# Kernel optimization log

Measured on AMD Instinct MI355X. Metric: run time of the kernel, lower is better.

Reference implementation:

```python
import jax, jax.numpy as jnp
import numpy as np

NEG_INF = -1e30  # stand-in for float('-inf') that is softmax-safe


def setup_inputs() -> dict:
    key = jax.random.key(0)
    ks = jax.random.split(key, 6)
    B, H, S, D = 2, 8, 1024, 64
    NF, K = 4, 3
    return {
        "query": jax.random.normal(ks[0], (B, H, S, D), dtype=jnp.float32),
        "keys": jax.random.normal(ks[1], (B, H, S, D), dtype=jnp.float32),
        "vals": jax.random.normal(ks[2], (B, H, S, D), dtype=jnp.float32),
        "mask": jnp.ones((B, 1, S, S), dtype=jnp.int32),
        "conv_w": jax.random.normal(ks[3], (NF, 1, K, K), dtype=jnp.float32) * (1.0 / K),
        "conv_b": jnp.zeros((NF,), dtype=jnp.float32),
        "lin_w": jax.random.normal(ks[4], (1, NF), dtype=jnp.float32) * 0.5,
        "lin_b": jnp.zeros((1,), dtype=jnp.float32),
    }


def reference(query, keys, vals, mask, conv_w, conv_b, lin_w, lin_b):
    B, H, S, D = query.shape
    NF = conv_w.shape[0]
    K = conv_w.shape[2]
    scale = jnp.asarray(D, query.dtype) ** 0.5

    # [B,H,S,S] raw dot-product scores
    dp = jnp.einsum("bhsd,bhtd->bhst", query, keys) / scale

    # conv2d over the score matrix: treat (B*H) as batch, 1 input channel
    x = dp.reshape(B * H, 1, S, S)
    conv = jax.lax.conv_general_dilated(
        x, conv_w,
        window_strides=(1, 1),
        padding=[(K // 2, K // 2), (K // 2, K // 2)],
        dimension_numbers=("NCHW", "OIHW", "NCHW"),
    ) + conv_b[None, :, None, None]
    conv = jax.nn.leaky_relu(conv, negative_slope=0.01)  # [B*H, NF, S, S]

    # per-pixel linear over the filter axis (Linear(num_filters, 1))
    conv = conv.reshape(B, H, NF, S, S)
    preattn = jnp.einsum("bhfst,f->bhst", conv, lin_w[0]) + lin_b[0]

    # masking + softmax (mask broadcasts over heads)
    preattn = jnp.where(mask == 0, jnp.asarray(NEG_INF, preattn.dtype), preattn)
    attn = jax.nn.softmax(preattn, axis=-1)

    # dropout is identity in eval mode
    return jnp.einsum("bhst,bhtd->bhsd", attn, vals)
```

## Files before the change

kernel.cpp:

```cpp
#include <hip/hip_runtime.h>
#include <math.h>

#define S_LEN 1024
#define D_DIM 64
#define NBH   16

typedef unsigned short ushort_t;
typedef __attribute__((ext_vector_type(8))) short short8;
typedef __attribute__((ext_vector_type(4))) short short4v;
typedef __attribute__((ext_vector_type(4))) float f32x4;
typedef __attribute__((ext_vector_type(2))) float f32x2;

__device__ __forceinline__ ushort_t rne_bf16(float x) {
    unsigned u = __float_as_uint(x);
    return (ushort_t)((u + 0x7FFFu + ((u >> 16) & 1u)) >> 16);
}
__device__ __forceinline__ void split1(float x, ushort_t& h, ushort_t& l) {
    h = rne_bf16(x);
    float hf = __uint_as_float((unsigned)h << 16);
    l = rne_bf16(x - hf);
}

__global__ __launch_bounds__(256) void prep(
    const float* __restrict__ k, const float* __restrict__ v,
    const int* __restrict__ mask,
    ushort_t* __restrict__ khi, ushort_t* __restrict__ klo,
    ushort_t* __restrict__ vhi, ushort_t* __restrict__ vlo,
    unsigned* __restrict__ mw)
{
    __shared__ float Ls[64][65];
    const int tid = threadIdx.x;
    const int bx = blockIdx.x;
    if (bx < 512) {
        const int gid  = bx * 256 + tid;
        const int bh   = gid >> 13;
        const int tile = (gid >> 7) & 63;
        const int ch   = (gid >> 6) & 1;
        const int lane = gid & 63;
        const int quad = lane >> 4, t15 = lane & 15;
        const float* src = k + ((size_t)bh * S_LEN + tile * 16 + t15) * D_DIM
                             + ch * 32 + quad * 8;
        float x[8];
        *(float4*)(x + 0) = *(const float4*)(src);
        *(float4*)(x + 4) = *(const float4*)(src + 4);
        short8 hv, lv;
        #pragma unroll
        for (int i = 0; i < 8; ++i) {
            ushort_t h, l;
            split1(x[i], h, l);
            hv[i] = (short)h; lv[i] = (short)l;
        }
        *(short8*)(khi + (size_t)gid * 8) = hv;
        *(short8*)(klo + (size_t)gid * 8) = lv;
    } else if (bx < 768) {
        const int bi = bx - 512;
        const int tt = bi & 15, bh = bi >> 4;
        const float* vb = v + ((size_t)bh * S_LEN + tt * 64) * D_DIM;
        #pragma unroll
        for (int p = 0; p < 4; ++p) {
            int idx = p * 1024 + tid * 4;
            int r = idx >> 6, c = idx & 63;
            float4 x = *(const float4*)(vb + r * 64 + c);
            Ls[r][c] = x.x; Ls[r][c+1] = x.y; Ls[r][c+2] = x.z; Ls[r][c+3] = x.w;
        }
        __syncthreads();
        const int d = tid >> 2, c0 = (tid & 3) * 16;
        ushort_t hi[16], lo[16];
        #pragma unroll
        for (int j = 0; j < 16; ++j) split1(Ls[c0 + j][d], hi[j], lo[j]);
        const int tb0 = tt * 8 + (c0 >> 3);
        const size_t o0 = (((size_t)bh * 128 + tb0) * 64 + d) * 8;
        const size_t o1 = (((size_t)bh * 128 + tb0 + 1) * 64 + d) * 8;
        *(short8*)(vhi + o0) = *(short8*)(hi);
        *(short8*)(vhi + o1) = *(short8*)(hi + 8);
        *(short8*)(vlo + o0) = *(short8*)(lo);
        *(short8*)(vlo + o1) = *(short8*)(lo + 8);
    } else {
        const int gid = (bx - 768) * 256 + tid;
        const int row = gid >> 5, wd = gid & 31;
        const int4* mp = (const int4*)(mask + (size_t)row * 1024 + wd * 32);
        unsigned bits = 0;
        #pragma unroll
        for (int p = 0; p < 8; ++p) {
            int4 qv = mp[p];
            bits |= (qv.x != 0 ? 1u : 0u) << (p * 4 + 0);
            bits |= (qv.y != 0 ? 1u : 0u) << (p * 4 + 1);
            bits |= (qv.z != 0 ? 1u : 0u) << (p * 4 + 2);
            bits |= (qv.w != 0 ? 1u : 0u) << (p * 4 + 3);
        }
        mw[(size_t)row * 32 + wd] = bits;
    }
}

__global__ __launch_bounds__(256) void qk_mfma(
    const float* __restrict__ q,
    const ushort_t* __restrict__ khi, const ushort_t* __restrict__ klo,
    float* __restrict__ dp)
{
    const int strip = blockIdx.x, st = blockIdx.y, bh = blockIdx.z;
    const int s0 = st * 16;
    const int tid = threadIdx.x;
    const int wave = tid >> 6, lane = tid & 63;
    const int m = lane & 15, quad = lane >> 4;

    const float* qp = q + ((size_t)bh * S_LEN + s0 + m) * D_DIM + quad * 8;
    float qa[16];
    *(float4*)(qa + 0)  = *(const float4*)(qp + 0);
    *(float4*)(qa + 4)  = *(const float4*)(qp + 4);
    *(float4*)(qa + 8)  = *(const float4*)(qp + 32);
    *(float4*)(qa + 12) = *(const float4*)(qp + 36);
    short8 ahi0, alo0, ahi1, alo1;
    #pragma unroll
    for (int i = 0; i < 8; ++i) {
        ushort_t h, l;
        split1(qa[i], h, l);      ahi0[i] = (short)h; alo0[i] = (short)l;
        split1(qa[8 + i], h, l);  ahi1[i] = (short)h; alo1[i] = (short)l;
    }

    const int tile0 = strip * 16 + wave * 4;
    float* dpb = dp + ((size_t)bh * S_LEN + s0) * S_LEN;
    #pragma unroll
    for (int tt = 0; tt < 4; ++tt) {
        const int tile = tile0 + tt;
        const size_t kb = ((size_t)bh * 8192 + tile * 128) + lane;
        short8 bhi0 = *(const short8*)(khi + kb * 8);
        short8 blo0 = *(const short8*)(klo + kb * 8);
        short8 bhi1 = *(const short8*)(khi + (kb + 64) * 8);
        short8 blo1 = *(const short8*)(klo + (kb + 64) * 8);
        f32x4 acc = {0.f, 0.f, 0.f, 0.f};
        acc = __builtin_amdgcn_mfma_f32_16x16x32_bf16(ahi0, bhi0, acc, 0, 0, 0);
        acc = __builtin_amdgcn_mfma_f32_16x16x32_bf16(ahi0, blo0, acc, 0, 0, 0);
        acc = __builtin_amdgcn_mfma_f32_16x16x32_bf16(alo0, bhi0, acc, 0, 0, 0);
        acc = __builtin_amdgcn_mfma_f32_16x16x32_bf16(ahi1, bhi1, acc, 0, 0, 0);
        acc = __builtin_amdgcn_mfma_f32_16x16x32_bf16(ahi1, blo1, acc, 0, 0, 0);
        acc = __builtin_amdgcn_mfma_f32_16x16x32_bf16(alo1, bhi1, acc, 0, 0, 0);
        const int t0 = tile * 16;
        #pragma unroll
        for (int r = 0; r < 4; ++r)
            dpb[(size_t)(quad * 4 + r) * S_LEN + t0 + m] = acc[r] * 0.125f;
    }
}

#define BUFS 1032
#define PSTR 1040
__global__ __launch_bounds__(512) void conv_av(
    const float* __restrict__ dp, const unsigned* __restrict__ mw,
    const ushort_t* __restrict__ vhi, const ushort_t* __restrict__ vlo,
    const float* __restrict__ conv_w, const float* __restrict__ conv_b,
    const float* __restrict__ lin_w, const float* __restrict__ lin_b,
    float* __restrict__ out)
{
    __shared__ float buf[10 * BUFS];
    __shared__ ushort_t pP[16 * PSTR];
    __shared__ float oBuf[16][68];
    __shared__ float lS[16];

    const int st = blockIdx.x, bh = blockIdx.y;
    const int s0 = st * 16;
    const int b  = bh >> 3;
    const int tid = threadIdx.x;
    const int wave = tid >> 6, lane = tid & 63;
    const int m = lane & 15, quad = lane >> 4;

    float w[36];
    #pragma unroll
    for (int i = 0; i < 36; ++i) w[i] = conv_w[i];
    float cb[4], lw[4];
    #pragma unroll
    for (int f = 0; f < 4; ++f) { cb[f] = conv_b[f]; lw[f] = lin_w[f]; }
    const float lb = lin_b[0];

    const float* base = dp + (size_t)bh * S_LEN * S_LEN;

    #pragma unroll
    for (int phase = 0; phase < 2; ++phase) {
        const int sbase = s0 - 1 + phase * 8;
        #pragma unroll
        for (int it = 0; it < 5; ++it) {
            const int idx = it * 512 + tid;
            const int row = idx >> 8, c4 = idx & 255;
            const int sr = sbase + row;
            float4 val = make_float4(0.f, 0.f, 0.f, 0.f);
            if (sr >= 0 && sr < S_LEN)
                val = *(const float4*)(base + (size_t)sr * S_LEN + c4 * 4);
            *(float4*)&buf[row * BUFS + c4 * 4] = val;
        }
        if (tid < 80) buf[(tid >> 3) * BUFS + 1024 + (tid & 7)] = 0.f;
        __syncthreads();

        const int r = phase * 8 + wave;
        const int srow = s0 + r;
        float ls = 0.f;
        #pragma unroll
        for (int g = 0; g < 4; ++g) {
            const int c0 = lane * 4 + 256 * g;
            const int li = c0 ? c0 - 1 : 1028;
            float vv[3][6];
            #pragma unroll
            for (int dr = 0; dr < 3; ++dr) {
                const float* rp = &buf[(wave + dr) * BUFS];
                f32x4 md = *(const f32x4*)(rp + c0);
                vv[dr][0] = rp[li];
                vv[dr][1] = md.x; vv[dr][2] = md.y; vv[dr][3] = md.z; vv[dr][4] = md.w;
                vv[dr][5] = rp[c0 + 4];
            }
            f32x2 pa = {lb, lb}, pb = {lb, lb};
            #pragma unroll
            for (int f = 0; f < 4; ++f) {
                f32x2 ca = {cb[f], cb[f]}, cbv = ca;
                #pragma unroll
                for (int dr = 0; dr < 3; ++dr) {
                    #pragma unroll
                    for (int dc = 0; dc < 3; ++dc) {
                        const float wt = w[f * 9 + dr * 3 + dc];
                        f32x2 ia = {vv[dr][dc],     vv[dr][dc + 1]};
                        f32x2 ib = {vv[dr][dc + 2], vv[dr][dc + 3]};
                        ca  += wt * ia;
                        cbv += wt * ib;
                    }
                }
                f32x2 la  = {fmaxf(ca.x, 0.f)  + 0.01f * fminf(ca.x, 0.f),
                             fmaxf(ca.y, 0.f)  + 0.01f * fminf(ca.y, 0.f)};
                f32x2 lb2 = {fmaxf(cbv.x, 0.f) + 0.01f * fminf(cbv.x, 0.f),
                             fmaxf(cbv.y, 0.f) + 0.01f * fminf(cbv.y, 0.f)};
                pa += lw[f] * la;
                pb += lw[f] * lb2;
            }
            const unsigned word = mw[((size_t)b * S_LEN + srow) * 32 + (lane >> 3) + 8 * g];
            const unsigned nib  = (word >> ((lane & 7) * 4)) & 0xFu;
            float pre[4] = {pa.x, pa.y, pb.x, pb.y};
            #pragma unroll
            for (int i = 0; i < 4; ++i)
                if (!((nib >> i) & 1u)) pre[i] = -1e30f;
            float pv[4];
            #pragma unroll
            for (int i = 0; i < 4; ++i) { pv[i] = __expf(pre[i]); ls += pv[i]; }
            short4v hv = {(short)rne_bf16(pv[0]), (short)rne_bf16(pv[1]),
                          (short)rne_bf16(pv[2]), (short)rne_bf16(pv[3])};
            *(short4v*)&pP[r * PSTR + c0] = hv;
        }
        #pragma unroll
        for (int off = 1; off < 64; off <<= 1) ls += __shfl_xor(ls, off);
        if (lane == 0) lS[r] = ls;
        __syncthreads();
    }

    const int d0 = (wave & 3) * 16;
    const int th = wave >> 2;
    f32x4 O = {0.f, 0.f, 0.f, 0.f};
    #pragma unroll 4
    for (int i = 0; i < 16; ++i) {
        const int c = th * 16 + i;
        short8 ph = *(const short8*)&pP[m * PSTR + c * 32 + quad * 8];
        const size_t vb = (((size_t)bh * 128 + c * 4 + quad) * 64 + d0 + m) * 8;
        short8 vh = *(const short8*)(vhi + vb);
        short8 vl = *(const short8*)(vlo + vb);
        O = __builtin_amdgcn_mfma_f32_16x16x32_bf16(ph, vh, O, 0, 0, 0);
        O = __builtin_amdgcn_mfma_f32_16x16x32_bf16(ph, vl, O, 0, 0, 0);
    }
    if (wave < 4) {
        #pragma unroll
        for (int r = 0; r < 4; ++r) oBuf[quad * 4 + r][d0 + m] = O[r];
    }
    __syncthreads();
    if (wave >= 4) {
        #pragma unroll
        for (int r = 0; r < 4; ++r) {
            const int br = quad * 4 + r;
            out[((size_t)bh * S_LEN + s0 + br) * D_DIM + d0 + m] =
                (O[r] + oBuf[br][d0 + m]) / lS[br];
        }
    }
}

extern "C" void kernel_launch(void* const* d_in, const int* in_sizes, int n_in,
                              void* d_out, int out_size, void* d_ws, size_t ws_size,
                              hipStream_t stream) {
    const float* q      = (const float*)d_in[0];
    const float* k      = (const float*)d_in[1];
    const float* v      = (const float*)d_in[2];
    const int*   mask   = (const int*)d_in[3];
    const float* conv_w = (const float*)d_in[4];
    const float* conv_b = (const float*)d_in[5];
    const float* lin_w  = (const float*)d_in[6];
    const float* lin_b  = (const float*)d_in[7];
    float* out = (float*)d_out;

    char* wsb = (char*)d_ws;
    const size_t MB = 1024 * 1024;
    ushort_t* khi  = (ushort_t*)(wsb + 0 * MB);
    ushort_t* klo  = (ushort_t*)(wsb + 2 * MB);
    ushort_t* vhi  = (ushort_t*)(wsb + 4 * MB);
    ushort_t* vlo  = (ushort_t*)(wsb + 6 * MB);
    unsigned* mw   = (unsigned*)(wsb + 8 * MB);
    float*    dp   = (float*)(wsb + 16 * MB);

    prep<<<dim3(1024), 256, 0, stream>>>(k, v, mask, khi, klo, vhi, vlo, mw);
    qk_mfma<<<dim3(4, 64, NBH), 256, 0, stream>>>(q, khi, klo, dp);
    conv_av<<<dim3(64, NBH), 512, 0, stream>>>(
        dp, mw, vhi, vlo, conv_w, conv_b, lin_w, lin_b, out);
}
```

Baseline: 142.0 us.

## Fuse K split into QK kernel, stage score stores, register-tile conv reads

The K bf16 hi/lo split moves out of the prep kernel and into qk_mfma, which now loads fp32 K directly. That removes the khi/klo workspace round trip and shrinks the prep grid. qk_mfma stages each wave's score tile in LDS so global writes become coalesced float4 rows instead of scattered scalar stores. conv_av drops the large shared-memory row buffer: each thread loads a 6x6 register window straight from global and computes four output rows. The mask words are preloaded into LDS, and row sums are reduced via per-wave partials instead of per-phase barriers. This trades LDS usage and barriers for redundant global and cache reads of overlapping rows, plus higher register pressure.

```diff
diff --git a/kernel.cpp b/kernel.cpp
--- a/kernel.cpp
+++ b/kernel.cpp
@@ -22,39 +22,15 @@
 }
 
 __global__ __launch_bounds__(256) void prep(
-    const float* __restrict__ k, const float* __restrict__ v,
-    const int* __restrict__ mask,
-    ushort_t* __restrict__ khi, ushort_t* __restrict__ klo,
+    const float* __restrict__ v, const int* __restrict__ mask,
     ushort_t* __restrict__ vhi, ushort_t* __restrict__ vlo,
     unsigned* __restrict__ mw)
 {
     __shared__ float Ls[64][65];
     const int tid = threadIdx.x;
     const int bx = blockIdx.x;
-    if (bx < 512) {
-        const int gid  = bx * 256 + tid;
-        const int bh   = gid >> 13;
-        const int tile = (gid >> 7) & 63;
-        const int ch   = (gid >> 6) & 1;
-        const int lane = gid & 63;
-        const int quad = lane >> 4, t15 = lane & 15;
-        const float* src = k + ((size_t)bh * S_LEN + tile * 16 + t15) * D_DIM
-                             + ch * 32 + quad * 8;
-        float x[8];
-        *(float4*)(x + 0) = *(const float4*)(src);
-        *(float4*)(x + 4) = *(const float4*)(src + 4);
-        short8 hv, lv;
-        #pragma unroll
-        for (int i = 0; i < 8; ++i) {
-            ushort_t h, l;
-            split1(x[i], h, l);
-            hv[i] = (short)h; lv[i] = (short)l;
-        }
-        *(short8*)(khi + (size_t)gid * 8) = hv;
-        *(short8*)(klo + (size_t)gid * 8) = lv;
-    } else if (bx < 768) {
-        const int bi = bx - 512;
-        const int tt = bi & 15, bh = bi >> 4;
+    if (bx < 256) {
+        const int tt = bx & 15, bh = bx >> 4;
         const float* vb = v + ((size_t)bh * S_LEN + tt * 64) * D_DIM;
         #pragma unroll
         for (int p = 0; p < 4; ++p) {
@@ -76,7 +52,7 @@
         *(short8*)(vlo + o0) = *(short8*)(lo);
         *(short8*)(vlo + o1) = *(short8*)(lo + 8);
     } else {
-        const int gid = (bx - 768) * 256 + tid;
+        const int gid = (bx - 256) * 256 + tid;
         const int row = gid >> 5, wd = gid & 31;
         const int4* mp = (const int4*)(mask + (size_t)row * 1024 + wd * 32);
         unsigned bits = 0;
@@ -93,10 +69,10 @@
 }
 
 __global__ __launch_bounds__(256) void qk_mfma(
-    const float* __restrict__ q,
-    const ushort_t* __restrict__ khi, const ushort_t* __restrict__ klo,
+    const float* __restrict__ q, const float* __restrict__ k,
     float* __restrict__ dp)
 {
+    __shared__ float Ls[4][16][68];
     const int strip = blockIdx.x, st = blockIdx.y, bh = blockIdx.z;
     const int s0 = st * 16;
     const int tid = threadIdx.x;
@@ -119,14 +95,23 @@
 
     const int tile0 = strip * 16 + wave * 4;
     float* dpb = dp + ((size_t)bh * S_LEN + s0) * S_LEN;
+
     #pragma unroll
     for (int tt = 0; tt < 4; ++tt) {
-        const int tile = tile0 + tt;
-        const size_t kb = ((size_t)bh * 8192 + tile * 128) + lane;
-        short8 bhi0 = *(const short8*)(khi + kb * 8);
-        short8 blo0 = *(const short8*)(klo + kb * 8);
-        short8 bhi1 = *(const short8*)(khi + (kb + 64) * 8);
-        short8 blo1 = *(const short8*)(klo + (kb + 64) * 8);
+        const int t0 = (tile0 + tt) * 16;
+        const float* kp = k + ((size_t)bh * S_LEN + t0 + m) * D_DIM + quad * 8;
+        float kb[16];
+        *(float4*)(kb + 0)  = *(const float4*)(kp + 0);
+        *(float4*)(kb + 4)  = *(const float4*)(kp + 4);
+        *(float4*)(kb + 8)  = *(const float4*)(kp + 32);
+        *(float4*)(kb + 12) = *(const float4*)(kp + 36);
+        short8 bhi0, blo0, bhi1, blo1;
+        #pragma unroll
+        for (int i = 0; i < 8; ++i) {
+            ushort_t h, l;
+            split1(kb[i], h, l);      bhi0[i] = (short)h; blo0[i] = (short)l;
+            split1(kb[8 + i], h, l);  bhi1[i] = (short)h; blo1[i] = (short)l;
+        }
         f32x4 acc = {0.f, 0.f, 0.f, 0.f};
         acc = __builtin_amdgcn_mfma_f32_16x16x32_bf16(ahi0, bhi0, acc, 0, 0, 0);
         acc = __builtin_amdgcn_mfma_f32_16x16x32_bf16(ahi0, blo0, acc, 0, 0, 0);
@@ -134,15 +119,21 @@
         acc = __builtin_amdgcn_mfma_f32_16x16x32_bf16(ahi1, bhi1, acc, 0, 0, 0);
         acc = __builtin_amdgcn_mfma_f32_16x16x32_bf16(ahi1, blo1, acc, 0, 0, 0);
         acc = __builtin_amdgcn_mfma_f32_16x16x32_bf16(alo1, bhi1, acc, 0, 0, 0);
-        const int t0 = tile * 16;
         #pragma unroll
         for (int r = 0; r < 4; ++r)
-            dpb[(size_t)(quad * 4 + r) * S_LEN + t0 + m] = acc[r] * 0.125f;
-    }
-}
-
-#define BUFS 1032
-#define PSTR 1040
+            Ls[wave][quad * 4 + r][tt * 16 + m] = acc[r] * 0.125f;
+    }
+    const int cb = strip * 256 + wave * 64;
+    #pragma unroll
+    for (int p = 0; p < 4; ++p) {
+        const int row = p * 4 + (lane >> 4);
+        const int f4  = lane & 15;
+        float4 val = *(const float4*)&Ls[wave][row][f4 * 4];
+        *(float4*)&dpb[(size_t)row * S_LEN + cb + f4 * 4] = val;
+    }
+}
+
+#define PSTR 1048
 __global__ __launch_bounds__(512) void conv_av(
     const float* __restrict__ dp, const unsigned* __restrict__ mw,
     const ushort_t* __restrict__ vhi, const ushort_t* __restrict__ vlo,
@@ -150,10 +141,10 @@
     const float* __restrict__ lin_w, const float* __restrict__ lin_b,
     float* __restrict__ out)
 {
-    __shared__ float buf[10 * BUFS];
     __shared__ ushort_t pP[16 * PSTR];
     __shared__ float oBuf[16][68];
-    __shared__ float lS[16];
+    __shared__ float lsPart[16][4];
+    __shared__ unsigned mb[16][32];
 
     const int st = blockIdx.x, bh = blockIdx.y;
     const int s0 = st * 16;
@@ -162,6 +153,11 @@
     const int wave = tid >> 6, lane = tid & 63;
     const int m = lane & 15, quad = lane >> 4;
 
+    {
+        const int row = tid >> 5, wd = tid & 31;
+        mb[row][wd] = mw[((size_t)b * S_LEN + s0 + row) * 32 + wd];
+    }
+
     float w[36];
     #pragma unroll
     for (int i = 0; i < 36; ++i) w[i] = conv_w[i];
@@ -170,51 +166,45 @@
     for (int f = 0; f < 4; ++f) { cb[f] = conv_b[f]; lw[f] = lin_w[f]; }
     const float lb = lin_b[0];
 
-    const float* base = dp + (size_t)bh * S_LEN * S_LEN;
-
-    #pragma unroll
-    for (int phase = 0; phase < 2; ++phase) {
-        const int sbase = s0 - 1 + phase * 8;
-        #pragma unroll
-        for (int it = 0; it < 5; ++it) {
-            const int idx = it * 512 + tid;
-            const int row = idx >> 8, c4 = idx & 255;
-            const int sr = sbase + row;
-            float4 val = make_float4(0.f, 0.f, 0.f, 0.f);
-            if (sr >= 0 && sr < S_LEN)
-                val = *(const float4*)(base + (size_t)sr * S_LEN + c4 * 4);
-            *(float4*)&buf[row * BUFS + c4 * 4] = val;
-        }
-        if (tid < 80) buf[(tid >> 3) * BUFS + 1024 + (tid & 7)] = 0.f;
-        __syncthreads();
-
-        const int r = phase * 8 + wave;
-        const int srow = s0 + r;
-        float ls = 0.f;
-        #pragma unroll
-        for (int g = 0; g < 4; ++g) {
-            const int c0 = lane * 4 + 256 * g;
-            const int li = c0 ? c0 - 1 : 1028;
-            float vv[3][6];
-            #pragma unroll
-            for (int dr = 0; dr < 3; ++dr) {
-                const float* rp = &buf[(wave + dr) * BUFS];
-                f32x4 md = *(const f32x4*)(rp + c0);
-                vv[dr][0] = rp[li];
-                vv[dr][1] = md.x; vv[dr][2] = md.y; vv[dr][3] = md.z; vv[dr][4] = md.w;
-                vv[dr][5] = rp[c0 + 4];
+    const int rh = tid >> 8, cg = tid & 255, c0 = cg * 4;
+    const float* dpb = dp + (size_t)bh * S_LEN * S_LEN;
+    __syncthreads();
+
+    #pragma unroll
+    for (int pass = 0; pass < 2; ++pass) {
+        const int obase = rh * 8 + pass * 4;
+        float rowv[6][6];
+        #pragma unroll
+        for (int jj = 0; jj < 6; ++jj) {
+            const int ir = s0 + obase - 1 + jj;
+            if (ir >= 0 && ir < S_LEN) {
+                const float* rp = dpb + (size_t)ir * S_LEN + c0;
+                f32x4 md = *(const f32x4*)rp;
+                rowv[jj][0] = cg ? rp[-1] : 0.f;
+                rowv[jj][1] = md.x; rowv[jj][2] = md.y;
+                rowv[jj][3] = md.z; rowv[jj][4] = md.w;
+                rowv[jj][5] = (cg < 255) ? rp[4] : 0.f;
+            } else {
+                #pragma unroll
+                for (int i = 0; i < 6; ++i) rowv[jj][i] = 0.f;
             }
+        }
+        float ls[4];
+        #pragma unroll
+        for (int jo = 0; jo < 4; ++jo) {
+            const int o = obase + jo;
             f32x2 pa = {lb, lb}, pb = {lb, lb};
             #pragma unroll
             for (int f = 0; f < 4; ++f) {
                 f32x2 ca = {cb[f], cb[f]}, cbv = ca;
                 #pragma unroll
                 for (int dr = 0; dr < 3; ++dr) {
+                    const float* vv = rowv[jo + dr];
                     #pragma unroll
                     for (int dc = 0; dc < 3; ++dc) {
                         const float wt = w[f * 9 + dr * 3 + dc];
-                        f32x2 ia = {vv[dr][dc],     vv[dr][dc + 1]};
-                        f32x2 ib = {vv[dr][dc + 2], vv[dr][dc + 3]};
+                        f32x2 ia = {vv[dc],     vv[dc + 1]};
+                        f32x2 ib = {vv[dc + 2], vv[dc + 3]};
                         ca  += wt * ia;
                         cbv += wt * ib;
                     }
@@ -226,24 +216,29 @@
                 pa += lw[f] * la;
                 pb += lw[f] * lb2;
             }
-            const unsigned word = mw[((size_t)b * S_LEN + srow) * 32 + (lane >> 3) + 8 * g];
-            const unsigned nib  = (word >> ((lane & 7) * 4)) & 0xFu;
+            const unsigned word = mb[o][cg >> 3];
+            const unsigned nib  = (word >> ((cg & 7) * 4)) & 0xFu;
             float pre[4] = {pa.x, pa.y, pb.x, pb.y};
             #pragma unroll
             for (int i = 0; i < 4; ++i)
                 if (!((nib >> i) & 1u)) pre[i] = -1e30f;
             float pv[4];
             #pragma unroll
-            for (int i = 0; i < 4; ++i) { pv[i] = __expf(pre[i]); ls += pv[i]; }
+            for (int i = 0; i < 4; ++i) pv[i] = __expf(pre[i]);
+            ls[jo] = (pv[0] + pv[1]) + (pv[2] + pv[3]);
             short4v hv = {(short)rne_bf16(pv[0]), (short)rne_bf16(pv[1]),
                           (short)rne_bf16(pv[2]), (short)rne_bf16(pv[3])};
-            *(short4v*)&pP[r * PSTR + c0] = hv;
-        }
-        #pragma unroll
-        for (int off = 1; off < 64; off <<= 1) ls += __shfl_xor(ls, off);
-        if (lane == 0) lS[r] = ls;
-        __syncthreads();
-    }
+            *(short4v*)&pP[o * PSTR + c0] = hv;
+        }
+        #pragma unroll
+        for (int jo = 0; jo < 4; ++jo) {
+            float t = ls[jo];
+            #pragma unroll
+            for (int off = 1; off < 64; off <<= 1) t += __shfl_xor(t, off);
+            if (lane == 0) lsPart[obase + jo][wave & 3] = t;
+        }
+    }
+    __syncthreads();
 
     const int d0 = (wave & 3) * 16;
     const int th = wave >> 2;
@@ -267,8 +262,10 @@
         #pragma unroll
         for (int r = 0; r < 4; ++r) {
             const int br = quad * 4 + r;
+            const float lsum = (lsPart[br][0] + lsPart[br][1]) +
+                               (lsPart[br][2] + lsPart[br][3]);
             out[((size_t)bh * S_LEN + s0 + br) * D_DIM + d0 + m] =
-                (O[r] + oBuf[br][d0 + m]) / lS[br];
+                (O[r] + oBuf[br][d0 + m]) / lsum;
         }
     }
 }
@@ -288,15 +285,13 @@
 
     char* wsb = (char*)d_ws;
     const size_t MB = 1024 * 1024;
-    ushort_t* khi  = (ushort_t*)(wsb + 0 * MB);
-    ushort_t* klo  = (ushort_t*)(wsb + 2 * MB);
-    ushort_t* vhi  = (ushort_t*)(wsb + 4 * MB);
-    ushort_t* vlo  = (ushort_t*)(wsb + 6 * MB);
-    unsigned* mw   = (unsigned*)(wsb + 8 * MB);
-    float*    dp   = (float*)(wsb + 16 * MB);
-
-    prep<<<dim3(1024), 256, 0, stream>>>(k, v, mask, khi, klo, vhi, vlo, mw);
-    qk_mfma<<<dim3(4, 64, NBH), 256, 0, stream>>>(q, khi, klo, dp);
+    ushort_t* vhi = (ushort_t*)(wsb + 0 * MB);
+    ushort_t* vlo = (ushort_t*)(wsb + 2 * MB);
+    unsigned* mw  = (unsigned*)(wsb + 4 * MB);
+    float*    dp  = (float*)(wsb + 16 * MB);
+
+    prep<<<dim3(512), 256, 0, stream>>>(v, mask, vhi, vlo, mw);
+    qk_mfma<<<dim3(4, 64, NBH), 256, 0, stream>>>(q, k, dp);
     conv_av<<<dim3(64, NBH), 512, 0, stream>>>(
         dp, mw, vhi, vlo, conv_w, conv_b, lin_w, lin_b, out);
 }
```

New measurement: 156.4 us. 10.1% more time.
